# Optimization experiments

Measured on AMD Instinct MI355X. Metric: run time of the kernel, lower is better.

Reference implementation:

```python
import jax, jax.numpy as jnp
import numpy as np


def setup_inputs() -> dict:
    key = jax.random.key(0)
    k1, k2, k3 = jax.random.split(key, 3)
    N, Cin, Cout, K, H, W = 8, 32, 32, 3, 64, 64
    x = jax.random.normal(k1, (N, Cin, H, W), dtype=jnp.float32)
    # spatially-varying filter bank: one (Cout, Cin, K, K) filter per output pixel
    weight = jax.random.normal(k2, (Cout, Cin, K, K, H, W), dtype=jnp.float32) * 0.05
    bias = jax.random.normal(k3, (Cout, 1, 1), dtype=jnp.float32)
    return {"x": x, "weight": weight, "bias": bias}


def reference(x, weight, bias):
    # x: (N, Cin, H, W); weight: (Cout, Cin, K, K, H, W); bias: (Cout, 1, 1)
    Cout, Cin, K, _, H, W = weight.shape
    p = K // 2  # 'same' padding, as in F.pad(x, (p,p,p,p))
    xp = jnp.pad(x, ((0, 0), (0, 0), (p, p), (p, p)))
    # Extract K*K shifted views; ordering (Cin-major, then kh, kw) matches
    # torch.nn.functional.unfold's channel layout used by weight.view(Cout, Cin*K*K, H*W).
    patches = jnp.stack(
        [xp[:, :, i:i + H, j:j + W] for i in range(K) for j in range(K)],
        axis=2,
    )  # (N, Cin, K*K, H, W)
    w = weight.reshape(Cout, Cin, K * K, H, W)
    # per-pixel weighted reduction over (Cin, K*K)
    out = jnp.einsum('ncphw,ocphw->nohw', patches, w)  # (N, Cout, H, W)
    return out + bias
```

## Files before the change

### kernel.cpp

```cpp
#include <hip/hip_runtime.h>


#define Nn 8
#define CI 32
#define CO 32
#define Hh 64
#define Ww 64
#define HW 4096

__global__ __launch_bounds__(64) void svconv_kernel(
    const float* __restrict__ x, const float* __restrict__ wgt,
    const float* __restrict__ bias, float* __restrict__ out) {
  int t = blockIdx.x * 64 + threadIdx.x;
  int wb = t & 31;
  int h  = (t >> 5) & 63;
  int o  = t >> 11;
  int w0 = wb << 1;

  float acc0[Nn], acc1[Nn];
  #pragma unroll
  for (int n = 0; n < Nn; ++n) { acc0[n] = 0.f; acc1[n] = 0.f; }

  const float* wq = wgt + (size_t)(o * CI * 9) * HW + h * Ww + w0;

  const bool c0 = (w0 >= 1);
  const bool c3 = (w0 + 2 < Ww);
  const int  i0 = c0 ? (w0 - 1) : 0;
  const int  i3 = c3 ? (w0 + 2) : (Ww - 1);

  #pragma unroll 2
  for (int ci = 0; ci < CI; ++ci) {
    #pragma unroll
    for (int kh = 0; kh < 3; ++kh) {
      int  ih = h + kh - 1;
      bool rv = ((unsigned)ih < (unsigned)Hh);
      int  ihc = rv ? ih : 0;
      const float* xr = x + ci * HW + ihc * Ww;

      float2 wv0 = *(const float2*)(wq);
      float2 wv1 = *(const float2*)(wq + HW);
      float2 wv2 = *(const float2*)(wq + 2 * HW);
      wq += 3 * HW;

      #pragma unroll
      for (int n = 0; n < Nn; ++n) {
        const float* xrn = xr + n * (CI * HW);
        float xv0 = (rv && c0) ? xrn[i0]     : 0.f;
        float xv1 = rv         ? xrn[w0]     : 0.f;
        float xv2 = rv         ? xrn[w0 + 1] : 0.f;
        float xv3 = (rv && c3) ? xrn[i3]     : 0.f;
        acc0[n] = fmaf(wv0.x, xv0, acc0[n]);
        acc0[n] = fmaf(wv1.x, xv1, acc0[n]);
        acc0[n] = fmaf(wv2.x, xv2, acc0[n]);
        acc1[n] = fmaf(wv0.y, xv1, acc1[n]);
        acc1[n] = fmaf(wv1.y, xv2, acc1[n]);
        acc1[n] = fmaf(wv2.y, xv3, acc1[n]);
      }
    }
  }

  float b = bias[o];
  size_t obase = (size_t)o * HW + (size_t)h * Ww + w0;
  #pragma unroll
  for (int n = 0; n < Nn; ++n) {
    float2 r;
    r.x = acc0[n] + b;
    r.y = acc1[n] + b;
    *(float2*)(out + (size_t)n * (CO * HW) + obase) = r;
  }
}

extern "C" void kernel_launch(void* const* d_in, const int* in_sizes, int n_in,
                              void* d_out, int out_size, void* d_ws, size_t ws_size,
                              hipStream_t stream) {
  const float* x    = (const float*)d_in[0];
  const float* wgt  = (const float*)d_in[1];
  const float* bias = (const float*)d_in[2];
  float* out = (float*)d_out;

  dim3 grid(65536 / 64), block(64);
  svconv_kernel<<<grid, block, 0, stream>>>(x, wgt, bias, out);
}
```

Measured before the change: 289.0 us.

## Split input-channel reduction across four waves and use lane shuffles for halos

```diff
diff --git a/kernel.cpp b/kernel.cpp
--- a/kernel.cpp
+++ b/kernel.cpp
@@ -7,66 +7,87 @@
 #define Hh 64
 #define Ww 64
 #define HW 4096
+#define SPLITS 4
+#define CIPS 8
 
-__global__ __launch_bounds__(64) void svconv_kernel(
+__global__ __launch_bounds__(256, 4) void svconv_kernel(
     const float* __restrict__ x, const float* __restrict__ wgt,
     const float* __restrict__ bias, float* __restrict__ out) {
-  int t = blockIdx.x * 64 + threadIdx.x;
-  int wb = t & 31;
-  int h  = (t >> 5) & 63;
-  int o  = t >> 11;
-  int w0 = wb << 1;
+  __shared__ float lds[SPLITS][64][17];
+
+  const int tid  = threadIdx.x;
+  const int s    = tid >> 6;
+  const int lane = tid & 63;
+  const int hrow = lane >> 5;
+  const int wb   = lane & 31;
+  const int w0   = wb << 1;
+  const int o     = blockIdx.x >> 5;
+  const int hbase = (blockIdx.x & 31) << 1;
+  const int h     = hbase + hrow;
 
   float acc0[Nn], acc1[Nn];
   #pragma unroll
   for (int n = 0; n < Nn; ++n) { acc0[n] = 0.f; acc1[n] = 0.f; }
 
-  const float* wq = wgt + (size_t)(o * CI * 9) * HW + h * Ww + w0;
+  const bool c0 = (wb > 0);
+  const bool c3 = (wb < 31);
 
-  const bool c0 = (w0 >= 1);
-  const bool c3 = (w0 + 2 < Ww);
-  const int  i0 = c0 ? (w0 - 1) : 0;
-  const int  i3 = c3 ? (w0 + 2) : (Ww - 1);
+  const float* wq = wgt + ((size_t)(o * CI + s * CIPS) * 9) * HW + h * Ww + w0;
 
   #pragma unroll 2
-  for (int ci = 0; ci < CI; ++ci) {
+  for (int ci8 = 0; ci8 < CIPS; ++ci8) {
+    const int ci = s * CIPS + ci8;
+
+    float2 wv[3][3];
+    #pragma unroll
+    for (int kh = 0; kh < 3; ++kh)
+      #pragma unroll
+      for (int kw = 0; kw < 3; ++kw)
+        wv[kh][kw] = *(const float2*)(wq + (kh * 3 + kw) * HW);
+    wq += 9 * HW;
+
     #pragma unroll
     for (int kh = 0; kh < 3; ++kh) {
-      int  ih = h + kh - 1;
-      bool rv = ((unsigned)ih < (unsigned)Hh);
-      int  ihc = rv ? ih : 0;
-      const float* xr = x + ci * HW + ihc * Ww;
-
-      float2 wv0 = *(const float2*)(wq);
-      float2 wv1 = *(const float2*)(wq + HW);
-      float2 wv2 = *(const float2*)(wq + 2 * HW);
-      wq += 3 * HW;
+      const int  ih = h + kh - 1;
+      const bool rv = ((unsigned)ih < (unsigned)Hh);
+      const int  ihc = rv ? ih : 0;
+      const float* xr = x + ci * HW + ihc * Ww + w0;
 
       #pragma unroll
       for (int n = 0; n < Nn; ++n) {
-        const float* xrn = xr + n * (CI * HW);
-        float xv0 = (rv && c0) ? xrn[i0]     : 0.f;
-        float xv1 = rv         ? xrn[w0]     : 0.f;
-        float xv2 = rv         ? xrn[w0 + 1] : 0.f;
-        float xv3 = (rv && c3) ? xrn[i3]     : 0.f;
-        acc0[n] = fmaf(wv0.x, xv0, acc0[n]);
-        acc0[n] = fmaf(wv1.x, xv1, acc0[n]);
-        acc0[n] = fmaf(wv2.x, xv2, acc0[n]);
-        acc1[n] = fmaf(wv0.y, xv1, acc1[n]);
-        acc1[n] = fmaf(wv1.y, xv2, acc1[n]);
-        acc1[n] = fmaf(wv2.y, xv3, acc1[n]);
+        float2 v = *(const float2*)(xr + n * (CI * HW));
+        v.x = rv ? v.x : 0.f;
+        v.y = rv ? v.y : 0.f;
+        float xv0 = __shfl_up(v.y, 1, 64);
+        xv0 = c0 ? xv0 : 0.f;
+        float xv3 = __shfl_down(v.x, 1, 64);
+        xv3 = c3 ? xv3 : 0.f;
+        acc0[n] = fmaf(wv[kh][0].x, xv0, acc0[n]);
+        acc0[n] = fmaf(wv[kh][1].x, v.x, acc0[n]);
+        acc0[n] = fmaf(wv[kh][2].x, v.y, acc0[n]);
+        acc1[n] = fmaf(wv[kh][0].y, v.x, acc1[n]);
+        acc1[n] = fmaf(wv[kh][1].y, v.y, acc1[n]);
+        acc1[n] = fmaf(wv[kh][2].y, xv3, acc1[n]);
       }
     }
   }
 
-  float b = bias[o];
-  size_t obase = (size_t)o * HW + (size_t)h * Ww + w0;
   #pragma unroll
   for (int n = 0; n < Nn; ++n) {
-    float2 r;
-    r.x = acc0[n] + b;
-    r.y = acc1[n] + b;
-    *(float2*)(out + (size_t)n * (CO * HW) + obase) = r;
+    lds[s][lane][2 * n]     = acc0[n];
+    lds[s][lane][2 * n + 1] = acc1[n];
+  }
+  __syncthreads();
+
+  const int p  = tid & 63;
+  const int kq = tid >> 6;
+  const float b = bias[o];
+  #pragma unroll
+  for (int i = 0; i < 4; ++i) {
+    const int k = kq * 4 + i;
+    const float sum = lds[0][p][k] + lds[1][p][k] + lds[2][p][k] + lds[3][p][k];
+    const int n = k >> 1, pix = k & 1;
+    out[(size_t)(n * CO + o) * HW + (hbase + (p >> 5)) * Ww + (p & 31) * 2 + pix] = sum + b;
   }
 }
 
@@ -78,6 +99,6 @@
   const float* bias = (const float*)d_in[2];
   float* out = (float*)d_out;
 
-  dim3 grid(65536 / 64), block(64);
+  dim3 grid(1024), block(256);
   svconv_kernel<<<grid, block, 0, stream>>>(x, wgt, bias, out);
 }
```

After: 231.4 us. -20.0%, faster.

## Stage weights and input rows through double-buffered LDS with 256-thread blocks

Applied to the files above, without the earlier changes.

```diff
diff --git a/kernel.cpp b/kernel.cpp
--- a/kernel.cpp
+++ b/kernel.cpp
@@ -8,65 +8,115 @@
 #define Ww 64
 #define HW 4096
 
-__global__ __launch_bounds__(64) void svconv_kernel(
+__global__ __launch_bounds__(256, 4) void svconv_kernel(
     const float* __restrict__ x, const float* __restrict__ wgt,
     const float* __restrict__ bias, float* __restrict__ out) {
-  int t = blockIdx.x * 64 + threadIdx.x;
-  int wb = t & 31;
-  int h  = (t >> 5) & 63;
-  int o  = t >> 11;
-  int w0 = wb << 1;
+  __shared__ float w_lds[2][9][128];
+  __shared__ float x_lds[2][8][4][66];
 
-  float acc0[Nn], acc1[Nn];
-  #pragma unroll
-  for (int n = 0; n < Nn; ++n) { acc0[n] = 0.f; acc1[n] = 0.f; }
+  const int tid   = threadIdx.x;
+  const int o     = blockIdx.x >> 5;
+  const int hbase = (blockIdx.x & 31) << 1;
 
-  const float* wq = wgt + (size_t)(o * CI * 9) * HW + h * Ww + w0;
+  const int ws   = tid >> 6;
+  const int lane = tid & 63;
+  const int hrow = lane >> 5;
+  const int wp   = lane & 31;
+  const int w0   = wp << 1;
 
-  const bool c0 = (w0 >= 1);
-  const bool c3 = (w0 + 2 < Ww);
-  const int  i0 = c0 ? (w0 - 1) : 0;
-  const int  i3 = c3 ? (w0 + 2) : (Ww - 1);
+  const int  pA   = tid >> 5;
+  const int  qA   = tid & 31;
+  const bool hasB = (tid < 32);
+  const float* wgA = wgt + ((size_t)(o * CI * 9 + pA)) * HW + hbase * Ww + qA * 4;
+  const float* wgB = wgt + ((size_t)(o * CI * 9 + 8)) * HW + hbase * Ww + (tid & 31) * 4;
 
-  #pragma unroll 2
-  for (int ci = 0; ci < CI; ++ci) {
+  const int  nX0 = tid >> 6;
+  const int  nX1 = nX0 + 4;
+  const int  rX  = (tid >> 4) & 3;
+  const int  qX  = tid & 15;
+  const int  rgX = hbase - 1 + rX;
+  const bool okX = (rgX >= 0) && (rgX < Hh);
+  const int  rgc = okX ? rgX : 0;
+  const float* xg0 = x + (size_t)nX0 * CI * HW + rgc * Ww + qX * 4;
+  const float* xg1 = x + (size_t)nX1 * CI * HW + rgc * Ww + qX * 4;
+
+  if (tid < 128) {
+    const int b = tid >> 6, n = (tid >> 3) & 7, r = (tid >> 1) & 3, side = tid & 1;
+    x_lds[b][n][r][side ? 65 : 0] = 0.f;
+  }
+
+  float acc[2][2] = {{0.f, 0.f}, {0.f, 0.f}};
+  float4 vwA, vwB, vx0, vx1;
+
+  auto stage_issue = [&](int ci) {
+    const size_t cw = (size_t)ci * (9 * HW);
+    const size_t cx = (size_t)ci * HW;
+    vwA = *(const float4*)(wgA + cw);
+    if (hasB) vwB = *(const float4*)(wgB + cw);
+    vx0 = *(const float4*)(xg0 + cx);
+    vx1 = *(const float4*)(xg1 + cx);
+  };
+
+  auto stage_write = [&](int buf) {
+    *(float4*)&w_lds[buf][pA][qA * 4] = vwA;
+    if (hasB) *(float4*)&w_lds[buf][8][(tid & 31) * 4] = vwB;
+    float* d0 = &x_lds[buf][nX0][rX][1 + qX * 4];
+    d0[0] = okX ? vx0.x : 0.f;
+    d0[1] = okX ? vx0.y : 0.f;
+    d0[2] = okX ? vx0.z : 0.f;
+    d0[3] = okX ? vx0.w : 0.f;
+    float* d1 = &x_lds[buf][nX1][rX][1 + qX * 4];
+    d1[0] = okX ? vx1.x : 0.f;
+    d1[1] = okX ? vx1.y : 0.f;
+    d1[2] = okX ? vx1.z : 0.f;
+    d1[3] = okX ? vx1.w : 0.f;
+  };
+
+  auto compute = [&](int buf) {
+    float2 wv[9];
     #pragma unroll
-    for (int kh = 0; kh < 3; ++kh) {
-      int  ih = h + kh - 1;
-      bool rv = ((unsigned)ih < (unsigned)Hh);
-      int  ihc = rv ? ih : 0;
-      const float* xr = x + ci * HW + ihc * Ww;
-
-      float2 wv0 = *(const float2*)(wq);
-      float2 wv1 = *(const float2*)(wq + HW);
-      float2 wv2 = *(const float2*)(wq + 2 * HW);
-      wq += 3 * HW;
-
+    for (int p = 0; p < 9; ++p)
+      wv[p] = *(const float2*)&w_lds[buf][p][hrow * 64 + w0];
+    #pragma unroll
+    for (int nl = 0; nl < 2; ++nl) {
+      const int n = ws * 2 + nl;
       #pragma unroll
-      for (int n = 0; n < Nn; ++n) {
-        const float* xrn = xr + n * (CI * HW);
-        float xv0 = (rv && c0) ? xrn[i0]     : 0.f;
-        float xv1 = rv         ? xrn[w0]     : 0.f;
-        float xv2 = rv         ? xrn[w0 + 1] : 0.f;
-        float xv3 = (rv && c3) ? xrn[i3]     : 0.f;
-        acc0[n] = fmaf(wv0.x, xv0, acc0[n]);
-        acc0[n] = fmaf(wv1.x, xv1, acc0[n]);
-        acc0[n] = fmaf(wv2.x, xv2, acc0[n]);
-        acc1[n] = fmaf(wv0.y, xv1, acc1[n]);
-        acc1[n] = fmaf(wv1.y, xv2, acc1[n]);
-        acc1[n] = fmaf(wv2.y, xv3, acc1[n]);
+      for (int kh = 0; kh < 3; ++kh) {
+        float2 a = *(const float2*)&x_lds[buf][n][hrow + kh][w0];
+        float2 b = *(const float2*)&x_lds[buf][n][hrow + kh][w0 + 2];
+        acc[nl][0] = fmaf(wv[3 * kh + 0].x, a.x, acc[nl][0]);
+        acc[nl][0] = fmaf(wv[3 * kh + 1].x, a.y, acc[nl][0]);
+        acc[nl][0] = fmaf(wv[3 * kh + 2].x, b.x, acc[nl][0]);
+        acc[nl][1] = fmaf(wv[3 * kh + 0].y, a.y, acc[nl][1]);
+        acc[nl][1] = fmaf(wv[3 * kh + 1].y, b.x, acc[nl][1]);
+        acc[nl][1] = fmaf(wv[3 * kh + 2].y, b.y, acc[nl][1]);
       }
     }
+  };
+
+  stage_issue(0);
+  stage_write(0);
+  __syncthreads();
+
+  #pragma unroll 1
+  for (int ci = 0; ci < CI; ci += 2) {
+    stage_issue(ci + 1);
+    compute(0);
+    stage_write(1);
+    __syncthreads();
+    if (ci + 2 < CI) stage_issue(ci + 2);
+    compute(1);
+    if (ci + 2 < CI) stage_write(0);
+    __syncthreads();
   }
 
-  float b = bias[o];
-  size_t obase = (size_t)o * HW + (size_t)h * Ww + w0;
+  const float bo = bias[o];
   #pragma unroll
-  for (int n = 0; n < Nn; ++n) {
+  for (int nl = 0; nl < 2; ++nl) {
     float2 r;
-    r.x = acc0[n] + b;
-    r.y = acc1[n] + b;
-    *(float2*)(out + (size_t)n * (CO * HW) + obase) = r;
+    r.x = acc[nl][0] + bo;
+    r.y = acc[nl][1] + bo;
+    *(float2*)(out + ((size_t)(ws * 2 + nl) * CO + o) * HW + (hbase + hrow) * Ww + w0) = r;
   }
 }
 
@@ -78,6 +128,6 @@
   const float* bias = (const float*)d_in[2];
   float* out = (float*)d_out;
 
-  dim3 grid(65536 / 64), block(64);
+  dim3 grid(1024), block(256);
   svconv_kernel<<<grid, block, 0, stream>>>(x, wgt, bias, out);
 }
```

Measured after the change: 257.7 us. 10.8% less time.
